# Performance work log

Hardware: AMD Instinct MI355X
Metric: run time of the kernel (lower is better)

Reference implementation:

```python
import jax, jax.numpy as jnp
import numpy as np

WIN = 32            # window_size
LOW_TH, HIGH_TH = 5.0, 15.0  # density_thresholds


def _prelu(x, a):
    return jnp.where(x >= 0, x, a * x)


def _hist_density(x):
    B, _, N = x.shape
    i, q = x[:, 0], x[:, 1]
    scale = WIN / 4.0  # bins over range [-2, 2]
    ii = jnp.clip(jnp.floor((i + 2.0) * scale).astype(jnp.int32), 0, WIN - 1)
    qq = jnp.clip(jnp.floor((q + 2.0) * scale).astype(jnp.int32), 0, WIN - 1)
    valid = (i >= -2.0) & (i <= 2.0) & (q >= -2.0) & (q <= 2.0)
    boff = jnp.arange(B, dtype=jnp.int32)[:, None] * (WIN * WIN)
    flat = (boff + ii * WIN + qq).reshape(-1)
    H = jax.ops.segment_sum(valid.astype(jnp.float32).reshape(-1), flat,
                            num_segments=B * WIN * WIN).reshape(B, WIN, WIN)
    low = (H <= LOW_TH).astype(jnp.float32)
    med = ((H > LOW_TH) & (H <= HIGH_TH)).astype(jnp.float32)
    high = (H > HIGH_TH).astype(jnp.float32)
    return jnp.stack([high, med, low], axis=1)


def _conv(x, w, b, p):
    y = jax.lax.conv_general_dilated(x, w, (1, 1), [(p, p), (p, p)],
                                     dimension_numbers=('NCHW', 'OIHW', 'NCHW'))
    return y + b[None, :, None, None]


def _avgpool2(x):
    B, C, H, W = x.shape
    return x.reshape(B, C, H // 2, 2, W // 2, 2).mean(axis=(3, 5))


def setup_inputs():
    key = jax.random.key(0)
    ks = jax.random.split(key, 8)
    B, N = 4096, 1024
    x = jax.random.normal(ks[0], (B, 2, N), jnp.float32)

    def w(k, shape, fan_in):
        return jax.random.normal(k, shape, jnp.float32) * (1.0 / np.sqrt(fan_in))

    return {
        'x': x,
        'cw1': w(ks[1], (32, 3, 3, 3), 3 * 9),   'cb1': jnp.zeros(32, jnp.float32),  'a1': jnp.float32(0.25),
        'cw2': w(ks[2], (64, 32, 3, 3), 32 * 9),  'cb2': jnp.zeros(64, jnp.float32),  'a2': jnp.float32(0.25),
        'cw3': w(ks[3], (128, 64, 5, 5), 64 * 25),'cb3': jnp.zeros(128, jnp.float32), 'a3': jnp.float32(0.25),
        'fw1': w(ks[4], (256, 128 * 4 * 4), 128 * 4 * 4), 'fb1': jnp.zeros(256, jnp.float32), 'a4': jnp.float32(0.25),
        'fw2': w(ks[5], (128, 256), 256), 'fb2': jnp.zeros(128, jnp.float32),
    }


def reference(x, cw1, cb1, a1, cw2, cb2, a2, cw3, cb3, a3, fw1, fb1, a4, fw2, fb2):
    d = _hist_density(x)                              # [B, 3, 32, 32]
    h = _avgpool2(_prelu(_conv(d, cw1, cb1, 1), a1))  # [B, 32, 16, 16]
    h = _avgpool2(_prelu(_conv(h, cw2, cb2, 1), a2))  # [B, 64, 8, 8]
    h = _avgpool2(_prelu(_conv(h, cw3, cb3, 2), a3))  # [B, 128, 4, 4]
    # AdaptiveAvgPool2d((4,4)) is identity on 4x4; Dropout is identity in eval
    f = h.reshape(h.shape[0], -1)                     # [B, 2048]
    f = _prelu(f @ fw1.T + fb1, a4)                   # [B, 256]
    return f @ fw2.T + fb2                            # [B, 128]
```

## Files before the change

### kernel.cpp

```cpp
#include <hip/hip_runtime.h>
#include <hip/hip_bf16.h>
#include <cstdint>
#include <cstddef>

typedef short short8 __attribute__((ext_vector_type(8)));
typedef float f32x4 __attribute__((ext_vector_type(4)));
typedef float f32x16 __attribute__((ext_vector_type(16)));
typedef unsigned short u16x4 __attribute__((ext_vector_type(4)));

__device__ inline unsigned short f2b(float f) {
    union { __hip_bfloat16 h; unsigned short u; } cv;
    cv.h = __float2bfloat16(f);
    return cv.u;
}
__device__ inline float b2f(unsigned short u) {
    union { __hip_bfloat16 h; unsigned short u; } cv;
    cv.u = u;
    return __bfloat162float(cv.h);
}
__device__ inline float prelu(float v, float a) { return v >= 0.f ? v : a * v; }

__global__ void k_prep(const float* __restrict__ cw1,
                       const float* __restrict__ cw2,
                       const float* __restrict__ cw3,
                       const float* __restrict__ fw1,
                       const float* __restrict__ fw2,
                       unsigned short* __restrict__ cw1e,
                       unsigned short* __restrict__ cw2bf,
                       unsigned short* __restrict__ cw3bf,
                       unsigned short* __restrict__ fw1hi,
                       unsigned short* __restrict__ fw1lo,
                       float* __restrict__ fw2t)
{
    const int i = blockIdx.x * 256 + threadIdx.x;
    const int stride = gridDim.x * 256;
    if (i < 1024) {
        const int oc = i >> 5, k = i & 31;
        float v = 0.f;
        if (k < 27) { const int tap = k / 3, c = k - 3 * tap; v = cw1[oc * 27 + c * 9 + tap]; }
        cw1e[i] = f2b(v);
    }
    if (i < 18432) {
        const int tap = i >> 11, r = i & 2047, oc = r >> 5, ic = r & 31;
        cw2bf[i] = f2b(cw2[oc * 288 + ic * 9 + tap]);
    }
    for (int j = i; j < 204800; j += stride) {
        const int tap = j >> 13, r = j & 8191, oc = r >> 6, ic = r & 63;
        cw3bf[j] = f2b(cw3[oc * 1600 + ic * 25 + tap]);
    }
    for (int j = i; j < 524288; j += stride) {
        const int oc = j >> 11, k = j & 2047;
        const float w = fw1[j];
        const unsigned short hi = f2b(w);
        const unsigned short lo = f2b(w - b2f(hi));
        const size_t o = ((size_t)(k >> 3) * 256 + oc) * 8 + (k & 7);
        fw1hi[o] = hi; fw1lo[o] = lo;
    }
    for (int j = i; j < 32768; j += stride) {
        const int k = j >> 7, oc = j & 127;
        fw2t[j] = fw2[oc * 256 + k];
    }
}

__global__ __launch_bounds__(256) void k_convstack(
    const float* __restrict__ x,
    const unsigned short* __restrict__ cw1e, const float* __restrict__ cb1, const float* __restrict__ a1p,
    const unsigned short* __restrict__ cw2bf, const float* __restrict__ cb2, const float* __restrict__ a2p,
    const unsigned short* __restrict__ cw3bf, const float* __restrict__ cb3, const float* __restrict__ a3p,
    unsigned short* __restrict__ h3out)
{
    const int b0 = blockIdx.x * 2;
    const int t = threadIdx.x;
    const int wv = t >> 6;
    const int l  = t & 63;
    const int lx = l & 15;
    const int q  = l >> 4;

    __shared__ unsigned char  clsp[1156];
    __shared__ unsigned short h1p[256 * 40];
    __shared__ unsigned short h2p[2][64 * 72];
    int* hist = (int*)(&h2p[1][0]);

    const float a1 = *a1p, a2 = *a2p, a3 = *a3p;

    for (int half = 0; half < 2; ++half) {
        const int b = b0 + half;

        for (int i = t; i < 1024; i += 256) hist[i] = 0;
        for (int i = t; i < 1156; i += 256) clsp[i] = 255;
        __syncthreads();

        const float* xb = x + (size_t)b * 2048;
        for (int n = t; n < 1024; n += 256) {
            const float iv = xb[n];
            const float qv = xb[1024 + n];
            if (iv >= -2.f && iv <= 2.f && qv >= -2.f && qv <= 2.f) {
                int ii = (int)floorf((iv + 2.f) * 8.f);
                int qq = (int)floorf((qv + 2.f) * 8.f);
                ii = ii < 0 ? 0 : (ii > 31 ? 31 : ii);
                qq = qq < 0 ? 0 : (qq > 31 ? 31 : qq);
                atomicAdd(&hist[ii * 32 + qq], 1);
            }
        }
        __syncthreads();

        for (int i = t; i < 1024; i += 256) {
            const int H = hist[i];
            clsp[(i >> 5) * 34 + (i & 31) + 35] = (H > 15) ? 0 : ((H > 5) ? 1 : 2);
        }
        __syncthreads();

        {
            const int mt = wv & 1;
            const int yh = wv >> 1;
            const short8 a1f = *(const short8*)(cw1e + (mt * 16 + lx) * 32 + q * 8);
            float b1r[4];
            #pragma unroll
            for (int r = 0; r < 4; ++r) b1r[r] = cb1[mt * 16 + q * 4 + r];

            for (int py = yh * 8; py < yh * 8 + 8; ++py) {
                f32x4 mac[4];
                #pragma unroll
                for (int d = 0; d < 4; ++d) {
                    const int y = 2 * py + (d >> 1);
                    const int xx = (d & 1) * 16 + lx;
                    short8 bf;
                    #pragma unroll
                    for (int j = 0; j < 8; ++j) {
                        const int k = q * 8 + j;
                        const int tap = (k * 43) >> 7;
                        const int c = k - 3 * tap;
                        const int ky = (tap * 43) >> 7;
                        const int kx = tap - 3 * ky;
                        const unsigned char cc = clsp[(y + ky) * 34 + (xx + kx)];
                        bf[j] = (k < 27 && cc == c) ? (short)0x3F80 : (short)0;
                    }
                    f32x4 z = {0.f, 0.f, 0.f, 0.f};
                    mac[d] = __builtin_amdgcn_mfma_f32_16x16x32_bf16(a1f, bf, z, 0, 0, 0);
                }
                #pragma unroll
                for (int hx = 0; hx < 2; ++hx) {
                    f32x4 u;
                    #pragma unroll
                    for (int r = 0; r < 4; ++r) {
                        float v0 = prelu(mac[hx][r] + b1r[r], a1);
                        float v1 = prelu(mac[2 + hx][r] + b1r[r], a1);
                        u[r] = v0 + v1;
                    }
                    #pragma unroll
                    for (int r = 0; r < 4; ++r) u[r] += __shfl_xor(u[r], 1);
                    if ((lx & 1) == 0) {
                        const int px = hx * 8 + (lx >> 1);
                        const int pos = py * 16 + px;
                        u16x4 pk;
                        #pragma unroll
                        for (int r = 0; r < 4; ++r) pk[r] = f2b(0.25f * u[r]);
                        *(u16x4*)(h1p + pos * 40 + mt * 16 + q * 4) = pk;
                    }
                }
            }
        }
        __syncthreads();

        {
            short8 a2f[9];
            #pragma unroll
            for (int tap = 0; tap < 9; ++tap)
                a2f[tap] = *(const short8*)(cw2bf + tap * 2048 + (wv * 16 + lx) * 32 + q * 8);
            float b2r[4];
            #pragma unroll
            for (int r = 0; r < 4; ++r) b2r[r] = cb2[wv * 16 + q * 4 + r];

            for (int py = 0; py < 8; ++py) {
                f32x4 acc0 = {0.f, 0.f, 0.f, 0.f}, acc1 = {0.f, 0.f, 0.f, 0.f};
                #pragma unroll
                for (int tap = 0; tap < 9; ++tap) {
                    const int ky = tap / 3, kx = tap % 3;
                    const int sx = lx + kx - 1;
                    const bool sxok = (unsigned)sx < 16u;
                    #pragma unroll
                    for (int dy = 0; dy < 2; ++dy) {
                        const int sy = 2 * py + dy + ky - 1;
                        if (sy >= 0 && sy < 16) {
                            short8 bf = {0, 0, 0, 0, 0, 0, 0, 0};
                            if (sxok) bf = *(const short8*)(h1p + (sy * 16 + sx) * 40 + q * 8);
                            if (dy == 0) acc0 = __builtin_amdgcn_mfma_f32_16x16x32_bf16(a2f[tap], bf, acc0, 0, 0, 0);
                            else         acc1 = __builtin_amdgcn_mfma_f32_16x16x32_bf16(a2f[tap], bf, acc1, 0, 0, 0);
                        }
                    }
                }
                f32x4 u;
                #pragma unroll
                for (int r = 0; r < 4; ++r) {
                    float v0 = prelu(acc0[r] + b2r[r], a2);
                    float v1 = prelu(acc1[r] + b2r[r], a2);
                    u[r] = v0 + v1;
                }
                #pragma unroll
                for (int r = 0; r < 4; ++r) u[r] += __shfl_xor(u[r], 1);
                if ((lx & 1) == 0) {
                    const int pos = py * 8 + (lx >> 1);
                    u16x4 pk;
                    #pragma unroll
                    for (int r = 0; r < 4; ++r) pk[r] = f2b(0.25f * u[r]);
                    *(u16x4*)(&h2p[half][pos * 72 + wv * 16 + q * 4]) = pk;
                }
            }
        }
        __syncthreads();
    }

    {
        const int col = l & 31;
        const int hi  = l >> 5;

        f32x16 acc[4];
        #pragma unroll
        for (int nt = 0; nt < 4; ++nt)
            #pragma unroll
            for (int r = 0; r < 16; ++r) acc[nt][r] = 0.f;

        const unsigned short* abase = cw3bf + (size_t)(wv * 32 + col) * 64 + hi * 8;

        short8 aC[4], aN[4];
        #pragma unroll
        for (int kk = 0; kk < 4; ++kk)
            aC[kk] = *(const short8*)(abase + kk * 16);

        for (int tap = 0; tap < 25; ++tap) {
            if (tap < 24) {
                const unsigned short* anext = abase + (tap + 1) * 8192;
                #pragma unroll
                for (int kk = 0; kk < 4; ++kk)
                    aN[kk] = *(const short8*)(anext + kk * 16);
            }
            const int ky = (tap * 13) >> 6;
            const int kx = tap - 5 * ky;
            #pragma unroll
            for (int nt = 0; nt < 4; ++nt) {
                const int bb  = nt >> 1;
                const int pos = (nt & 1) * 32 + col;
                const int sy  = (pos >> 3) + ky - 2;
                const int sx  = (pos & 7) + kx - 2;
                const bool ok = (unsigned)sy < 8u && (unsigned)sx < 8u;
                const int soff = (sy * 8 + sx) * 72 + hi * 8;
                #pragma unroll
                for (int kk = 0; kk < 4; ++kk) {
                    short8 bf = {0, 0, 0, 0, 0, 0, 0, 0};
                    if (ok) bf = *(const short8*)(&h2p[bb][soff + kk * 16]);
                    acc[nt] = __builtin_amdgcn_mfma_f32_32x32x16_bf16(aC[kk], bf, acc[nt], 0, 0, 0);
                }
            }
            #pragma unroll
            for (int kk = 0; kk < 4; ++kk) aC[kk] = aN[kk];
        }

        float b3r[16];
        #pragma unroll
        for (int r = 0; r < 16; ++r)
            b3r[r] = cb3[wv * 32 + (r & 3) + 8 * (r >> 2) + 4 * hi];

        #pragma unroll
        for (int nt = 0; nt < 4; ++nt) {
            f32x16 u;
            #pragma unroll
            for (int r = 0; r < 16; ++r) u[r] = prelu(acc[nt][r] + b3r[r], a3);
            #pragma unroll
            for (int r = 0; r < 16; ++r) u[r] += __shfl_xor(u[r], 1);
            #pragma unroll
            for (int r = 0; r < 16; ++r) u[r] += __shfl_xor(u[r], 8);
            if ((col & 9) == 0) {
                const int b  = b0 + (nt >> 1);
                const int oy = (nt & 1) * 2 + (col >> 4);
                const int ox = (col & 7) >> 1;
                #pragma unroll
                for (int r = 0; r < 16; ++r) {
                    const int oc = wv * 32 + (r & 3) + 8 * (r >> 2) + 4 * hi;
                    h3out[(size_t)b * 2048 + oc * 16 + oy * 4 + ox] = f2b(0.25f * u[r]);
                }
            }
        }
    }
}

__global__ __launch_bounds__(512) void k_fc(
    const unsigned short* __restrict__ fw1hi,
    const unsigned short* __restrict__ fw1lo,
    const unsigned short* __restrict__ h3,
    const float* __restrict__ fb1, const float* __restrict__ a4p,
    const float* __restrict__ fw2t, const float* __restrict__ fb2,
    float* __restrict__ out)
{
    const int t  = threadIdx.x;
    const int wv = t >> 6;
    const int l  = t & 63;
    const int lx = l & 15;
    const int q  = l >> 4;
    const int b0 = blockIdx.x * 32;

    __shared__ unsigned short Bs[32 * 128];
    __shared__ float fT[256 * 34];

    f32x4 acc[2][2];
    #pragma unroll
    for (int mt = 0; mt < 2; ++mt)
        #pragma unroll
        for (int bn = 0; bn < 2; ++bn) { f32x4 z = {0.f,0.f,0.f,0.f}; acc[mt][bn] = z; }

    const int srow  = t >> 4;
    const int scolb = (t & 15) << 4;
    const unsigned short* gsrc = h3 + (size_t)(b0 + srow) * 2048
                               + ((scolb ^ ((srow & 7) << 4)) >> 1);

    for (int kc = 0; kc < 2048; kc += 128) {
        __builtin_amdgcn_global_load_lds(
            (const __attribute__((address_space(1))) unsigned int*)(gsrc + kc),
            (__attribute__((address_space(3))) unsigned int*)(Bs + t * 8),
            16, 0, 0);
        __syncthreads();

        #pragma unroll
        for (int s = 0; s < 4; ++s) {
            const int kb = ((kc + s * 32) >> 3) + q;
            const short8 ah0 = *(const short8*)(fw1hi + ((size_t)kb * 256 + wv * 32 + lx) * 8);
            const short8 ah1 = *(const short8*)(fw1hi + ((size_t)kb * 256 + wv * 32 + 16 + lx) * 8);
            const short8 al0 = *(const short8*)(fw1lo + ((size_t)kb * 256 + wv * 32 + lx) * 8);
            const short8 al1 = *(const short8*)(fw1lo + ((size_t)kb * 256 + wv * 32 + 16 + lx) * 8);
            #pragma unroll
            for (int bn = 0; bn < 2; ++bn) {
                const int rr = bn * 16 + lx;
                const short8 bfr = *(const short8*)((const char*)Bs + rr * 256
                                    + ((s * 64 + q * 16) ^ ((rr & 7) << 4)));
                acc[0][bn] = __builtin_amdgcn_mfma_f32_16x16x32_bf16(ah0, bfr, acc[0][bn], 0, 0, 0);
                acc[1][bn] = __builtin_amdgcn_mfma_f32_16x16x32_bf16(ah1, bfr, acc[1][bn], 0, 0, 0);
                acc[0][bn] = __builtin_amdgcn_mfma_f32_16x16x32_bf16(al0, bfr, acc[0][bn], 0, 0, 0);
                acc[1][bn] = __builtin_amdgcn_mfma_f32_16x16x32_bf16(al1, bfr, acc[1][bn], 0, 0, 0);
            }
        }
        __syncthreads();
    }

    const float a4 = *a4p;
    #pragma unroll
    for (int mt = 0; mt < 2; ++mt) {
        #pragma unroll
        for (int r = 0; r < 4; ++r) {
            const int oc = wv * 32 + mt * 16 + q * 4 + r;
            const float bb2 = fb1[oc];
            #pragma unroll
            for (int bn = 0; bn < 2; ++bn) {
                float v = acc[mt][bn][r] + bb2;
                v = v >= 0.f ? v : a4 * v;
                fT[oc * 34 + bn * 16 + lx] = v;
            }
        }
    }
    __syncthreads();

    {
        const int oc2 = t & 127;
        const int bh  = t >> 7;
        float acc2[8];
        #pragma unroll
        for (int j = 0; j < 8; ++j) acc2[j] = 0.f;
        for (int k = 0; k < 256; ++k) {
            const float w = fw2t[k * 128 + oc2];
            const float* fr = &fT[k * 34 + bh * 8];
            #pragma unroll
            for (int j = 0; j < 8; ++j) acc2[j] += w * fr[j];
        }
        const float bb2 = fb2[oc2];
        #pragma unroll
        for (int j = 0; j < 8; ++j)
            out[(size_t)(b0 + bh * 8 + j) * 128 + oc2] = acc2[j] + bb2;
    }
}

extern "C" void kernel_launch(void* const* d_in, const int* in_sizes, int n_in,
                              void* d_out, int out_size, void* d_ws, size_t ws_size,
                              hipStream_t stream)
{
    const float* x   = (const float*)d_in[0];
    const float* cw1 = (const float*)d_in[1];
    const float* cb1 = (const float*)d_in[2];
    const float* a1  = (const float*)d_in[3];
    const float* cw2 = (const float*)d_in[4];
    const float* cb2 = (const float*)d_in[5];
    const float* a2  = (const float*)d_in[6];
    const float* cw3 = (const float*)d_in[7];
    const float* cb3 = (const float*)d_in[8];
    const float* a3  = (const float*)d_in[9];
    const float* fw1 = (const float*)d_in[10];
    const float* fb1 = (const float*)d_in[11];
    const float* a4  = (const float*)d_in[12];
    const float* fw2 = (const float*)d_in[13];
    const float* fb2 = (const float*)d_in[14];
    float* out = (float*)d_out;

    unsigned short* cw1e  = (unsigned short*)((char*)d_ws);
    unsigned short* cw2bf = (unsigned short*)((char*)d_ws + 2048);
    unsigned short* cw3bf = (unsigned short*)((char*)d_ws + 38912);
    unsigned short* fw1hi = (unsigned short*)((char*)d_ws + 448512);
    unsigned short* fw1lo = (unsigned short*)((char*)d_ws + 1497088);
    float*          fw2t  = (float*)((char*)d_ws + 2545664);
    unsigned short* h3    = (unsigned short*)((char*)d_ws + 2676736);

    const int B = in_sizes[0] / 2048;

    k_prep<<<800, 256, 0, stream>>>(cw1, cw2, cw3, fw1, fw2,
                                    cw1e, cw2bf, cw3bf, fw1hi, fw1lo, fw2t);
    k_convstack<<<B / 2, 256, 0, stream>>>(x, cw1e, cb1, a1, cw2bf, cb2, a2,
                                           cw3bf, cb3, a3, h3);
    k_fc<<<B / 32, 512, 0, stream>>>(fw1hi, fw1lo, h3, fb1, a4, fw2t, fb2, out);
}
```

Measured before the change: 300.3 us.

## Reassign wave work so each B fragment feeds two MFMA output tiles

```diff
diff --git a/kernel.cpp b/kernel.cpp
--- a/kernel.cpp
+++ b/kernel.cpp
@@ -111,15 +111,17 @@
         __syncthreads();
 
         {
-            const int mt = wv & 1;
-            const int yh = wv >> 1;
-            const short8 a1f = *(const short8*)(cw1e + (mt * 16 + lx) * 32 + q * 8);
-            float b1r[4];
-            #pragma unroll
-            for (int r = 0; r < 4; ++r) b1r[r] = cb1[mt * 16 + q * 4 + r];
-
-            for (int py = yh * 8; py < yh * 8 + 8; ++py) {
-                f32x4 mac[4];
+            const int yg = wv;
+            const short8 a1f0 = *(const short8*)(cw1e + lx * 32 + q * 8);
+            const short8 a1f1 = *(const short8*)(cw1e + (16 + lx) * 32 + q * 8);
+            float b1r[2][4];
+            #pragma unroll
+            for (int mt = 0; mt < 2; ++mt)
+                #pragma unroll
+                for (int r = 0; r < 4; ++r) b1r[mt][r] = cb1[mt * 16 + q * 4 + r];
+
+            for (int py = yg * 4; py < yg * 4 + 4; ++py) {
+                f32x4 mac[4][2];
                 #pragma unroll
                 for (int d = 0; d < 4; ++d) {
                     const int y = 2 * py + (d >> 1);
@@ -136,26 +138,30 @@
                         bf[j] = (k < 27 && cc == c) ? (short)0x3F80 : (short)0;
                     }
                     f32x4 z = {0.f, 0.f, 0.f, 0.f};
-                    mac[d] = __builtin_amdgcn_mfma_f32_16x16x32_bf16(a1f, bf, z, 0, 0, 0);
-                }
-                #pragma unroll
-                for (int hx = 0; hx < 2; ++hx) {
-                    f32x4 u;
-                    #pragma unroll
-                    for (int r = 0; r < 4; ++r) {
-                        float v0 = prelu(mac[hx][r] + b1r[r], a1);
-                        float v1 = prelu(mac[2 + hx][r] + b1r[r], a1);
-                        u[r] = v0 + v1;
-                    }
-                    #pragma unroll
-                    for (int r = 0; r < 4; ++r) u[r] += __shfl_xor(u[r], 1);
-                    if ((lx & 1) == 0) {
-                        const int px = hx * 8 + (lx >> 1);
-                        const int pos = py * 16 + px;
-                        u16x4 pk;
+                    mac[d][0] = __builtin_amdgcn_mfma_f32_16x16x32_bf16(a1f0, bf, z, 0, 0, 0);
+                    mac[d][1] = __builtin_amdgcn_mfma_f32_16x16x32_bf16(a1f1, bf, z, 0, 0, 0);
+                }
+                #pragma unroll
+                for (int mt = 0; mt < 2; ++mt) {
+                    #pragma unroll
+                    for (int hx = 0; hx < 2; ++hx) {
+                        f32x4 u;
                         #pragma unroll
-                        for (int r = 0; r < 4; ++r) pk[r] = f2b(0.25f * u[r]);
-                        *(u16x4*)(h1p + pos * 40 + mt * 16 + q * 4) = pk;
+                        for (int r = 0; r < 4; ++r) {
+                            float v0 = prelu(mac[hx][mt][r] + b1r[mt][r], a1);
+                            float v1 = prelu(mac[2 + hx][mt][r] + b1r[mt][r], a1);
+                            u[r] = v0 + v1;
+                        }
+                        #pragma unroll
+                        for (int r = 0; r < 4; ++r) u[r] += __shfl_xor(u[r], 1);
+                        if ((lx & 1) == 0) {
+                            const int px = hx * 8 + (lx >> 1);
+                            const int pos = py * 16 + px;
+                            u16x4 pk;
+                            #pragma unroll
+                            for (int r = 0; r < 4; ++r) pk[r] = f2b(0.25f * u[r]);
+                            *(u16x4*)(h1p + pos * 40 + mt * 16 + q * 4) = pk;
+                        }
                     }
                 }
             }
@@ -163,16 +169,27 @@
         __syncthreads();
 
         {
-            short8 a2f[9];
+            const int ob = wv & 1;
+            const int ph = wv >> 1;
+            short8 a2f[9][2];
             #pragma unroll
             for (int tap = 0; tap < 9; ++tap)
-                a2f[tap] = *(const short8*)(cw2bf + tap * 2048 + (wv * 16 + lx) * 32 + q * 8);
-            float b2r[4];
-            #pragma unroll
-            for (int r = 0; r < 4; ++r) b2r[r] = cb2[wv * 16 + q * 4 + r];
-
-            for (int py = 0; py < 8; ++py) {
-                f32x4 acc0 = {0.f, 0.f, 0.f, 0.f}, acc1 = {0.f, 0.f, 0.f, 0.f};
+                #pragma unroll
+                for (int mt = 0; mt < 2; ++mt)
+                    a2f[tap][mt] = *(const short8*)(cw2bf + tap * 2048 + (ob * 32 + mt * 16 + lx) * 32 + q * 8);
+            float b2r[2][4];
+            #pragma unroll
+            for (int mt = 0; mt < 2; ++mt)
+                #pragma unroll
+                for (int r = 0; r < 4; ++r) b2r[mt][r] = cb2[ob * 32 + mt * 16 + q * 4 + r];
+
+            for (int py = ph * 4; py < ph * 4 + 4; ++py) {
+                f32x4 acc[2][2];
+                #pragma unroll
+                for (int mt = 0; mt < 2; ++mt)
+                    #pragma unroll
+                    for (int dy = 0; dy < 2; ++dy) { f32x4 z = {0.f,0.f,0.f,0.f}; acc[mt][dy] = z; }
+
                 #pragma unroll
                 for (int tap = 0; tap < 9; ++tap) {
                     const int ky = tap / 3, kx = tap % 3;
@@ -184,26 +201,29 @@
                         if (sy >= 0 && sy < 16) {
                             short8 bf = {0, 0, 0, 0, 0, 0, 0, 0};
                             if (sxok) bf = *(const short8*)(h1p + (sy * 16 + sx) * 40 + q * 8);
-                            if (dy == 0) acc0 = __builtin_amdgcn_mfma_f32_16x16x32_bf16(a2f[tap], bf, acc0, 0, 0, 0);
-                            else         acc1 = __builtin_amdgcn_mfma_f32_16x16x32_bf16(a2f[tap], bf, acc1, 0, 0, 0);
+                            acc[0][dy] = __builtin_amdgcn_mfma_f32_16x16x32_bf16(a2f[tap][0], bf, acc[0][dy], 0, 0, 0);
+                            acc[1][dy] = __builtin_amdgcn_mfma_f32_16x16x32_bf16(a2f[tap][1], bf, acc[1][dy], 0, 0, 0);
                         }
                     }
                 }
-                f32x4 u;
-                #pragma unroll
-                for (int r = 0; r < 4; ++r) {
-                    float v0 = prelu(acc0[r] + b2r[r], a2);
-                    float v1 = prelu(acc1[r] + b2r[r], a2);
-                    u[r] = v0 + v1;
-                }
-                #pragma unroll
-                for (int r = 0; r < 4; ++r) u[r] += __shfl_xor(u[r], 1);
-                if ((lx & 1) == 0) {
-                    const int pos = py * 8 + (lx >> 1);
-                    u16x4 pk;
-                    #pragma unroll
-                    for (int r = 0; r < 4; ++r) pk[r] = f2b(0.25f * u[r]);
-                    *(u16x4*)(&h2p[half][pos * 72 + wv * 16 + q * 4]) = pk;
+                #pragma unroll
+                for (int mt = 0; mt < 2; ++mt) {
+                    f32x4 u;
+                    #pragma unroll
+                    for (int r = 0; r < 4; ++r) {
+                        float v0 = prelu(acc[mt][0][r] + b2r[mt][r], a2);
+                        float v1 = prelu(acc[mt][1][r] + b2r[mt][r], a2);
+                        u[r] = v0 + v1;
+                    }
+                    #pragma unroll
+                    for (int r = 0; r < 4; ++r) u[r] += __shfl_xor(u[r], 1);
+                    if ((lx & 1) == 0) {
+                        const int pos = py * 8 + (lx >> 1);
+                        u16x4 pk;
+                        #pragma unroll
+                        for (int r = 0; r < 4; ++r) pk[r] = f2b(0.25f * u[r]);
+                        *(u16x4*)(&h2p[half][pos * 72 + ob * 32 + mt * 16 + q * 4]) = pk;
+                    }
                 }
             }
         }
@@ -211,35 +231,42 @@
     }
 
     {
+        const int g  = wv & 1;
+        const int bc = wv >> 1;
         const int col = l & 31;
         const int hi  = l >> 5;
 
-        f32x16 acc[4];
-        #pragma unroll
-        for (int nt = 0; nt < 4; ++nt)
-            #pragma unroll
-            for (int r = 0; r < 16; ++r) acc[nt][r] = 0.f;
-
-        const unsigned short* abase = cw3bf + (size_t)(wv * 32 + col) * 64 + hi * 8;
-
-        short8 aC[4], aN[4];
-        #pragma unroll
-        for (int kk = 0; kk < 4; ++kk)
-            aC[kk] = *(const short8*)(abase + kk * 16);
+        f32x16 acc[2][2];
+        #pragma unroll
+        for (int mt = 0; mt < 2; ++mt)
+            #pragma unroll
+            for (int nt = 0; nt < 2; ++nt)
+                #pragma unroll
+                for (int r = 0; r < 16; ++r) acc[mt][nt][r] = 0.f;
+
+        const unsigned short* abase = cw3bf + (size_t)(g * 64 + col) * 64 + hi * 8;
+
+        short8 aC[2][4], aN[2][4];
+        #pragma unroll
+        for (int mt = 0; mt < 2; ++mt)
+            #pragma unroll
+            for (int kk = 0; kk < 4; ++kk)
+                aC[mt][kk] = *(const short8*)(abase + mt * 2048 + kk * 16);
 
         for (int tap = 0; tap < 25; ++tap) {
             if (tap < 24) {
                 const unsigned short* anext = abase + (tap + 1) * 8192;
                 #pragma unroll
-                for (int kk = 0; kk < 4; ++kk)
-                    aN[kk] = *(const short8*)(anext + kk * 16);
+                for (int mt = 0; mt < 2; ++mt)
+                    #pragma unroll
+                    for (int kk = 0; kk < 4; ++kk)
+                        aN[mt][kk] = *(const short8*)(anext + mt * 2048 + kk * 16);
             }
             const int ky = (tap * 13) >> 6;
             const int kx = tap - 5 * ky;
             #pragma unroll
-            for (int nt = 0; nt < 4; ++nt) {
-                const int bb  = nt >> 1;
-                const int pos = (nt & 1) * 32 + col;
+            for (int nt = 0; nt < 2; ++nt) {
+                const int pos = nt * 32 + col;
                 const int sy  = (pos >> 3) + ky - 2;
                 const int sx  = (pos & 7) + kx - 2;
                 const bool ok = (unsigned)sy < 8u && (unsigned)sx < 8u;
@@ -247,36 +274,41 @@
                 #pragma unroll
                 for (int kk = 0; kk < 4; ++kk) {
                     short8 bf = {0, 0, 0, 0, 0, 0, 0, 0};
-                    if (ok) bf = *(const short8*)(&h2p[bb][soff + kk * 16]);
-                    acc[nt] = __builtin_amdgcn_mfma_f32_32x32x16_bf16(aC[kk], bf, acc[nt], 0, 0, 0);
-                }
-            }
-            #pragma unroll
-            for (int kk = 0; kk < 4; ++kk) aC[kk] = aN[kk];
-        }
-
-        float b3r[16];
-        #pragma unroll
-        for (int r = 0; r < 16; ++r)
-            b3r[r] = cb3[wv * 32 + (r & 3) + 8 * (r >> 2) + 4 * hi];
-
-        #pragma unroll
-        for (int nt = 0; nt < 4; ++nt) {
-            f32x16 u;
-            #pragma unroll
-            for (int r = 0; r < 16; ++r) u[r] = prelu(acc[nt][r] + b3r[r], a3);
-            #pragma unroll
-            for (int r = 0; r < 16; ++r) u[r] += __shfl_xor(u[r], 1);
-            #pragma unroll
-            for (int r = 0; r < 16; ++r) u[r] += __shfl_xor(u[r], 8);
-            if ((col & 9) == 0) {
-                const int b  = b0 + (nt >> 1);
-                const int oy = (nt & 1) * 2 + (col >> 4);
-                const int ox = (col & 7) >> 1;
-                #pragma unroll
-                for (int r = 0; r < 16; ++r) {
-                    const int oc = wv * 32 + (r & 3) + 8 * (r >> 2) + 4 * hi;
-                    h3out[(size_t)b * 2048 + oc * 16 + oy * 4 + ox] = f2b(0.25f * u[r]);
+                    if (ok) bf = *(const short8*)(&h2p[bc][soff + kk * 16]);
+                    acc[0][nt] = __builtin_amdgcn_mfma_f32_32x32x16_bf16(aC[0][kk], bf, acc[0][nt], 0, 0, 0);
+                    acc[1][nt] = __builtin_amdgcn_mfma_f32_32x32x16_bf16(aC[1][kk], bf, acc[1][nt], 0, 0, 0);
+                }
+            }
+            #pragma unroll
+            for (int mt = 0; mt < 2; ++mt)
+                #pragma unroll
+                for (int kk = 0; kk < 4; ++kk) aC[mt][kk] = aN[mt][kk];
+        }
+
+        #pragma unroll
+        for (int mt = 0; mt < 2; ++mt) {
+            float b3r[16];
+            #pragma unroll
+            for (int r = 0; r < 16; ++r)
+                b3r[r] = cb3[g * 64 + mt * 32 + (r & 3) + 8 * (r >> 2) + 4 * hi];
+            #pragma unroll
+            for (int nt = 0; nt < 2; ++nt) {
+                f32x16 u;
+                #pragma unroll
+                for (int r = 0; r < 16; ++r) u[r] = prelu(acc[mt][nt][r] + b3r[r], a3);
+                #pragma unroll
+                for (int r = 0; r < 16; ++r) u[r] += __shfl_xor(u[r], 1);
+                #pragma unroll
+                for (int r = 0; r < 16; ++r) u[r] += __shfl_xor(u[r], 8);
+                if ((col & 9) == 0) {
+                    const int b  = b0 + bc;
+                    const int oy = nt * 2 + (col >> 4);
+                    const int ox = (col & 7) >> 1;
+                    #pragma unroll
+                    for (int r = 0; r < 16; ++r) {
+                        const int oc = g * 64 + mt * 32 + (r & 3) + 8 * (r >> 2) + 4 * hi;
+                        h3out[(size_t)b * 2048 + oc * 16 + oy * 4 + ox] = f2b(0.25f * u[r]);
+                    }
                 }
             }
         }
```

After: 353.1 us. 1.18x slower.
